# Kernel optimization log

Hardware: AMD Instinct MI355X
Metric: run time of the kernel (lower is better)

The kernel has to match this reference:

```python
import jax, jax.numpy as jnp
import numpy as np

EMBED = 1024
HEADS = 16
HEAD_DIM = EMBED // HEADS


def setup_inputs() -> dict:
    key = jax.random.key(0)
    ks = jax.random.split(key, 8)
    N, S, E = 4, 2048, EMBED
    s = 1.0 / np.sqrt(E)
    return {
        "values": jax.random.normal(ks[0], (N, S, E), jnp.float32),
        "keys": jax.random.normal(ks[1], (N, S, E), jnp.float32),
        "queries": jax.random.normal(ks[2], (N, S, E), jnp.float32),
        # nn.Linear weights stored as (out_features, in_features)
        "Wv": jax.random.normal(ks[3], (E, E), jnp.float32) * s,
        "Wk": jax.random.normal(ks[4], (E, E), jnp.float32) * s,
        "Wq": jax.random.normal(ks[5], (E, E), jnp.float32) * s,
        "Wo": jax.random.normal(ks[6], (E, E), jnp.float32) * s,
        "bo": jax.random.normal(ks[7], (E,), jnp.float32) * s,
    }


def reference(values, keys, queries, Wv, Wk, Wq, Wo, bo):
    N = queries.shape[0]
    H, D, E = HEADS, HEAD_DIM, EMBED
    # projections (torch Linear: x @ W.T), reshape to [N, S, H, D]
    v = (values @ Wv.T).reshape(N, -1, H, D)
    k = (keys @ Wk.T).reshape(N, -1, H, D)
    q = (queries @ Wq.T).reshape(N, -1, H, D)
    energy = jnp.einsum("nqhd,nkhd->nhqk", q, k)
    # NOTE: original scales by sqrt(embed_size), not sqrt(head_dim)
    attn = jax.nn.softmax(energy / jnp.sqrt(jnp.float32(E)), axis=3)
    out = jnp.einsum("nhql,nlhd->nqhd", attn, v).reshape(N, -1, H * D)
    return out @ Wo.T + bo
```

## Files before the change

### kernel.cpp

```cpp
#include <hip/hip_runtime.h>

typedef __bf16  bf16x8 __attribute__((ext_vector_type(8)));
typedef __bf16  bf16x4 __attribute__((ext_vector_type(4)));
typedef short   s16x4  __attribute__((ext_vector_type(4)));
typedef float   f32x4  __attribute__((ext_vector_type(4)));
typedef unsigned short u16x8 __attribute__((ext_vector_type(8)));

__device__ __forceinline__ unsigned short f2bf(float f) {
    union { float f; unsigned int u; } v; v.f = f;
    unsigned int u = v.u;
    unsigned int r = (u + 0x7fffu + ((u >> 16) & 1u)) >> 16;
    return (unsigned short)r;
}

__device__ __forceinline__ unsigned int pkbf(float lo, float hi) {
    union { float f; unsigned int u; } a, b; a.f = lo; b.f = hi;
    return __builtin_amdgcn_perm(b.u + 0x8000u, a.u + 0x8000u, 0x07060302u);
}

__device__ __forceinline__ void gld_lds16(const unsigned short* g, unsigned short* l) {
    auto gp = (const __attribute__((address_space(1))) unsigned int*)(const void*)g;
    auto lp = (__attribute__((address_space(3))) unsigned int*)(unsigned int)(unsigned long long)(void*)l;
    __builtin_amdgcn_global_load_lds(gp, lp, 16, 0, 0);
}

__device__ __forceinline__ f32x4 mfma16(bf16x4 a, bf16x4 b, f32x4 c) {
#if __has_builtin(__builtin_amdgcn_mfma_f32_16x16x16_bf16)
    return __builtin_amdgcn_mfma_f32_16x16x16_bf16(a, b, c, 0, 0, 0);
#elif __has_builtin(__builtin_amdgcn_mfma_f32_16x16x16bf16_1k)
    union U { bf16x4 h; s16x4 s; } ua, ub; ua.h = a; ub.h = b;
    return __builtin_amdgcn_mfma_f32_16x16x16bf16_1k(ua.s, ub.s, c, 0, 0, 0);
#else
    asm("v_mfma_f32_16x16x16_bf16 %0, %1, %2, %0" : "+v"(c) : "v"(a), "v"(b));
    return c;
#endif
}

__global__ void cast4_kernel(const float* __restrict__ a, const float* __restrict__ b,
                             const float* __restrict__ c, const float* __restrict__ d,
                             unsigned short* __restrict__ dst) {
    int sel = blockIdx.x >> 10;
    int off4 = (blockIdx.x & 1023) * 256 + threadIdx.x;
    const float* src = sel == 0 ? a : sel == 1 ? b : sel == 2 ? c : d;
    float4 f = ((const float4*)src)[off4];
    uint2 pk; pk.x = pkbf(f.x, f.y); pk.y = pkbf(f.z, f.w);
    ((uint2*)(dst + (size_t)sel * 1048576))[off4] = pk;
}

__global__ void cast_kernel(const float* __restrict__ src, unsigned short* __restrict__ dst, int n4) {
    int stride = gridDim.x * 256;
    for (int i = blockIdx.x * 256 + threadIdx.x; i < n4; i += stride) {
        float4 f = ((const float4*)src)[i];
        uint2 pk; pk.x = pkbf(f.x, f.y); pk.y = pkbf(f.z, f.w);
        ((uint2*)dst)[i] = pk;
    }
}

template <int MODE>
__global__ __launch_bounds__(256, 3)
void gemm_bt(const unsigned short* __restrict__ A, const unsigned short* __restrict__ Bt,
             void* __restrict__ dst, const float* __restrict__ bias, float a_scale)
{
    constexpr int K = 1024;
    __shared__ unsigned short As[2][4096];
    __shared__ unsigned short Bs[2][4096];

    const int t    = threadIdx.x;
    const int lane = t & 63;
    const int w    = t >> 6;
    const int q    = lane >> 4;
    const int ln   = lane & 15;
    const int wr   = w >> 1, wc = w & 1;
    const int m0   = blockIdx.x * 128;
    const int n0   = blockIdx.y * 128;
    const int srow = lane >> 2;
    const int scol = (lane & 3) * 8;

    f32x4 acc[4][4];
    const f32x4 zz = {0.f, 0.f, 0.f, 0.f};
#pragma unroll
    for (int i = 0; i < 4; ++i)
#pragma unroll
        for (int j = 0; j < 4; ++j) acc[i][j] = zz;

    auto stage = [&](int k0, int p) {
#pragma unroll
        for (int c = 0; c < 2; ++c) {
            int u = w * 2 + c;
            gld_lds16(A  + (size_t)(m0 + u * 16 + srow) * K + k0 + scol, &As[p][u * 512]);
            gld_lds16(Bt + (size_t)(n0 + u * 16 + srow) * K + k0 + scol, &Bs[p][u * 512]);
        }
    };

    stage(0, 0);
    for (int j = 0; j < 32; ++j) {
        __syncthreads();
        if (j < 31) stage((j + 1) * 32, (j + 1) & 1);
        const int p = j & 1;
        bf16x8 af[4], bfr[4];
#pragma unroll
        for (int i = 0; i < 4; ++i)
            af[i] = *(const bf16x8*)&As[p][(wr * 64 + i * 16 + ln) * 32 + q * 8];
#pragma unroll
        for (int jj = 0; jj < 4; ++jj)
            bfr[jj] = *(const bf16x8*)&Bs[p][(wc * 64 + jj * 16 + ln) * 32 + q * 8];
#pragma unroll
        for (int i = 0; i < 4; ++i)
#pragma unroll
            for (int jj = 0; jj < 4; ++jj)
                acc[i][jj] = __builtin_amdgcn_mfma_f32_16x16x32_bf16(af[i], bfr[jj], acc[i][jj], 0, 0, 0);
    }

#pragma unroll
    for (int i = 0; i < 4; ++i) {
#pragma unroll
        for (int j = 0; j < 4; ++j) {
            f32x4 c = acc[i][j];
            int mb = m0 + wr * 64 + i * 16 + q * 4;
            int nn = n0 + wc * 64 + j * 16 + ln;
            if constexpr (MODE == 1) {
                int b = mb >> 11, s = mb & 2047, h = nn >> 6, d = nn & 63;
                uint2 pk;
                pk.x = pkbf(c[0], c[1]);
                pk.y = pkbf(c[2], c[3]);
                size_t idx = (((size_t)(b * 16 + h) * 64) + d) * 2048 + s;
                *(uint2*)&((unsigned short*)dst)[idx] = pk;
            } else {
#pragma unroll
                for (int r = 0; r < 4; ++r) {
                    int m = mb + r;
                    float val = c[r] * a_scale;
                    if constexpr (MODE == 2) {
                        ((float*)dst)[(size_t)m * 1024 + nn] = val + bias[nn];
                    } else {
                        int b = m >> 11, s = m & 2047, h = nn >> 6, d = nn & 63;
                        size_t idx = (((size_t)(b * 16 + h) * 2048) + s) * 64 + d;
                        ((unsigned short*)dst)[idx] = f2bf(val);
                    }
                }
            }
        }
    }
}

__global__ __launch_bounds__(256, 4)
void attn_kernel(const unsigned short* __restrict__ Q, const unsigned short* __restrict__ Kg,
                 const unsigned short* __restrict__ Vt, unsigned short* __restrict__ Og)
{
    __shared__ __align__(16) unsigned short Ks[2][4096];
    __shared__ __align__(16) unsigned short Vs[2][4096];

    const int t    = threadIdx.x;
    const int lane = t & 63;
    const int w    = t >> 6;
    const int q    = lane >> 4;
    const int ln   = lane & 15;
    const int xs   = (ln >> 1) & 3;
    const int head = blockIdx.x;
    const int qt   = blockIdx.y;

    const unsigned short* Qh  = Q  + (size_t)head * 2048 * 64;
    const unsigned short* Kh  = Kg + (size_t)head * 2048 * 64;
    const unsigned short* Vth = Vt + (size_t)head * 64 * 2048;

    const int srow = lane >> 2;
    const int ssw  = ((lane & 3) ^ ((lane >> 3) & 3)) * 8;

    bf16x8 qf[2][2];
    const int rowb = qt * 128 + w * 32;
#pragma unroll
    for (int ti = 0; ti < 2; ++ti)
#pragma unroll
        for (int kc = 0; kc < 2; ++kc)
            qf[ti][kc] = *(const bf16x8*)&Qh[(size_t)(rowb + ti * 16 + ln) * 64 + kc * 32 + q * 8];

    const f32x4 zz = {0.f, 0.f, 0.f, 0.f};
    f32x4 oa[2][4];
#pragma unroll
    for (int ti = 0; ti < 2; ++ti)
#pragma unroll
        for (int dt = 0; dt < 4; ++dt) oa[ti][dt] = zz;
    float l_s[2] = {0.f, 0.f};

    auto stage = [&](int j, int p) {
#pragma unroll
        for (int c = 0; c < 2; ++c) {
            int u = w * 2 + c;
            int kc = u >> 2, rg = u & 3;
            gld_lds16(Kh + (size_t)(j * 64 + rg * 16 + srow) * 64 + kc * 32 + ssw,
                      &Ks[p][kc * 2048 + rg * 512]);
            gld_lds16(Vth + (size_t)(rg * 16 + srow) * 2048 + j * 64 + kc * 32 + ssw,
                      &Vs[p][kc * 2048 + rg * 512]);
        }
    };

    stage(0, 0);
    for (int j = 0; j < 32; ++j) {
        __syncthreads();
        if (j < 31) stage(j + 1, (j + 1) & 1);
        const int p = j & 1;

        bf16x4 pb[4][2];
        float rs0 = 0.f, rs1 = 0.f;
#pragma unroll
        for (int kt = 0; kt < 4; ++kt) {
            f32x4 s0 = zz, s1 = zz;
#pragma unroll
            for (int kc = 0; kc < 2; ++kc) {
                bf16x8 ka = *(const bf16x8*)&Ks[p][kc * 2048 + (kt * 16 + ln) * 32 + ((q ^ xs) * 8)];
                s0 = __builtin_amdgcn_mfma_f32_16x16x32_bf16(ka, qf[0][kc], s0, 0, 0, 0);
                s1 = __builtin_amdgcn_mfma_f32_16x16x32_bf16(ka, qf[1][kc], s1, 0, 0, 0);
            }
            {
                float a0 = exp2f(s0[0]), a1 = exp2f(s0[1]), a2 = exp2f(s0[2]), a3 = exp2f(s0[3]);
                rs0 += (a0 + a1) + (a2 + a3);
                f32x4 pe = {a0, a1, a2, a3};
                pb[kt][0] = __builtin_convertvector(pe, bf16x4);
            }
            {
                float b0 = exp2f(s1[0]), b1 = exp2f(s1[1]), b2 = exp2f(s1[2]), b3 = exp2f(s1[3]);
                rs1 += (b0 + b1) + (b2 + b3);
                f32x4 pe = {b0, b1, b2, b3};
                pb[kt][1] = __builtin_convertvector(pe, bf16x4);
            }
        }
        rs0 += __shfl_xor(rs0, 16); rs0 += __shfl_xor(rs0, 32); l_s[0] += rs0;
        rs1 += __shfl_xor(rs1, 16); rs1 += __shfl_xor(rs1, 32); l_s[1] += rs1;

#pragma unroll
        for (int kt = 0; kt < 4; ++kt) {
            const int kc = kt >> 1;
            const int so = ((((kt & 1) * 2 + (q >> 1)) ^ xs) * 8) + (q & 1) * 4;
            bf16x4 va[4];
#pragma unroll
            for (int dt = 0; dt < 4; ++dt)
                va[dt] = *(const bf16x4*)&Vs[p][kc * 2048 + (dt * 16 + ln) * 32 + so];
#pragma unroll
            for (int dt = 0; dt < 4; ++dt) {
                oa[0][dt] = mfma16(va[dt], pb[kt][0], oa[0][dt]);
                oa[1][dt] = mfma16(va[dt], pb[kt][1], oa[1][dt]);
            }
        }
    }

    const int n = head >> 4;
    const int hbase = (head & 15) * 64;
#pragma unroll
    for (int ti = 0; ti < 2; ++ti) {
        float inv = 1.f / l_s[ti];
        int sr = qt * 128 + w * 32 + ti * 16 + ln;
        size_t base = ((size_t)n * 2048 + sr) * 1024 + hbase;
#pragma unroll
        for (int dt = 0; dt < 4; ++dt) {
            uint2 pk;
            pk.x = pkbf(oa[ti][dt][0] * inv, oa[ti][dt][1] * inv);
            pk.y = pkbf(oa[ti][dt][2] * inv, oa[ti][dt][3] * inv);
            *(uint2*)&Og[base + dt * 16 + q * 4] = pk;
        }
    }
}

extern "C" void kernel_launch(void* const* d_in, const int* in_sizes, int n_in,
                              void* d_out, int out_size, void* d_ws, size_t ws_size,
                              hipStream_t stream)
{
    (void)in_sizes; (void)n_in; (void)out_size; (void)ws_size;
    const float* values  = (const float*)d_in[0];
    const float* keys    = (const float*)d_in[1];
    const float* queries = (const float*)d_in[2];
    const float* Wv = (const float*)d_in[3];
    const float* Wk = (const float*)d_in[4];
    const float* Wq = (const float*)d_in[5];
    const float* Wo = (const float*)d_in[6];
    const float* bo = (const float*)d_in[7];
    float* out = (float*)d_out;

    unsigned short* ws   = (unsigned short*)d_ws;
    unsigned short* Wv_b = ws;
    unsigned short* Wk_b = ws + 1048576;
    unsigned short* Wq_b = ws + 2097152;
    unsigned short* Wo_b = ws + 3145728;
    unsigned short* Act  = ws + 4194304;
    unsigned short* Ob   = Act;
    unsigned short* Qb   = ws + 12582912;
    unsigned short* Kb   = Qb + 8388608;
    unsigned short* Vtb  = Kb + 8388608;

    cast4_kernel<<<4096, 256, 0, stream>>>(Wv, Wk, Wq, Wo, ws);

    dim3 g(64, 8), b(256);
    const float qscale = 1.4426950408889634f / 32.f;

    cast_kernel<<<4096, 256, 0, stream>>>(values, Act, 2097152);
    gemm_bt<1><<<g, b, 0, stream>>>(Act, Wv_b, Vtb, nullptr, 1.f);
    cast_kernel<<<4096, 256, 0, stream>>>(keys, Act, 2097152);
    gemm_bt<0><<<g, b, 0, stream>>>(Act, Wk_b, Kb, nullptr, 1.f);
    cast_kernel<<<4096, 256, 0, stream>>>(queries, Act, 2097152);
    gemm_bt<0><<<g, b, 0, stream>>>(Act, Wq_b, Qb, nullptr, qscale);

    attn_kernel<<<dim3(64, 16), b, 0, stream>>>(Qb, Kb, Vtb, Ob);
    gemm_bt<2><<<g, b, 0, stream>>>(Ob, Wo_b, out, bo, 1.f);
}
```

Baseline: 367.6 us.

## Fuse fp32-to-bf16 activation casts into a single batched QKV projection GEMM

The three separate cast kernels and three projection GEMMs are replaced by one launch over a z-dimension of three. That kernel loads fp32 activations directly into registers and converts them to bf16 while staging into LDS, which removes the intermediate bf16 activation buffer and its round trip through memory. The attention kernel now uses the hardware exp2 builtin instead of exp2f, and it moves the cross-lane row-sum shuffles out of the inner loop so they run once at the end. In exchange, the A-operand path now goes through registers instead of the asynchronous global-to-LDS copy, which increases register pressure and may expose load latency.

Result: faster. 343.1 us (-6.7%).

```diff
diff --git a/kernel.cpp b/kernel.cpp
--- a/kernel.cpp
+++ b/kernel.cpp
@@ -4,7 +4,6 @@
 typedef __bf16  bf16x4 __attribute__((ext_vector_type(4)));
 typedef short   s16x4  __attribute__((ext_vector_type(4)));
 typedef float   f32x4  __attribute__((ext_vector_type(4)));
-typedef unsigned short u16x8 __attribute__((ext_vector_type(8)));
 
 __device__ __forceinline__ unsigned short f2bf(float f) {
     union { float f; unsigned int u; } v; v.f = f;
@@ -16,6 +15,14 @@
 __device__ __forceinline__ unsigned int pkbf(float lo, float hi) {
     union { float f; unsigned int u; } a, b; a.f = lo; b.f = hi;
     return __builtin_amdgcn_perm(b.u + 0x8000u, a.u + 0x8000u, 0x07060302u);
+}
+
+__device__ __forceinline__ float fexp2(float x) {
+#if __has_builtin(__builtin_amdgcn_exp2f)
+    return __builtin_amdgcn_exp2f(x);
+#else
+    float r; asm("v_exp_f32 %0, %1\n\ts_nop 1" : "=v"(r) : "v"(x)); return r;
+#endif
 }
 
 __device__ __forceinline__ void gld_lds16(const unsigned short* g, unsigned short* l) {
@@ -47,23 +54,21 @@
     ((uint2*)(dst + (size_t)sel * 1048576))[off4] = pk;
 }
 
-__global__ void cast_kernel(const float* __restrict__ src, unsigned short* __restrict__ dst, int n4) {
-    int stride = gridDim.x * 256;
-    for (int i = blockIdx.x * 256 + threadIdx.x; i < n4; i += stride) {
-        float4 f = ((const float4*)src)[i];
-        uint2 pk; pk.x = pkbf(f.x, f.y); pk.y = pkbf(f.z, f.w);
-        ((uint2*)dst)[i] = pk;
-    }
-}
-
-template <int MODE>
 __global__ __launch_bounds__(256, 3)
-void gemm_bt(const unsigned short* __restrict__ A, const unsigned short* __restrict__ Bt,
-             void* __restrict__ dst, const float* __restrict__ bias, float a_scale)
+void gemm_qkv(const float* __restrict__ V32, const float* __restrict__ K32,
+              const float* __restrict__ Q32, const unsigned short* __restrict__ W,
+              unsigned short* __restrict__ Vtb, unsigned short* __restrict__ Kb,
+              unsigned short* __restrict__ Qb, float qscale)
 {
     constexpr int K = 1024;
     __shared__ unsigned short As[2][4096];
     __shared__ unsigned short Bs[2][4096];
+
+    const int z = blockIdx.z;
+    const float* A32 = z == 0 ? V32 : z == 1 ? K32 : Q32;
+    const unsigned short* Bt = W + (size_t)z * 1048576;
+    unsigned short* dst = z == 0 ? Vtb : z == 1 ? Kb : Qb;
+    const float a_scale = z == 2 ? qscale : 1.f;
 
     const int t    = threadIdx.x;
     const int lane = t & 63;
@@ -83,6 +88,113 @@
 #pragma unroll
         for (int j = 0; j < 4; ++j) acc[i][j] = zz;
 
+    auto loadA = [&](int k0, float4* fa) {
+#pragma unroll
+        for (int c = 0; c < 2; ++c) {
+            int u = w * 2 + c;
+            const float* src = A32 + (size_t)(m0 + u * 16 + srow) * K + k0 + scol;
+            fa[c * 2]     = *(const float4*)src;
+            fa[c * 2 + 1] = *(const float4*)(src + 4);
+        }
+    };
+    auto writeA = [&](const float4* fa, int p) {
+#pragma unroll
+        for (int c = 0; c < 2; ++c) {
+            int u = w * 2 + c;
+            uint4 pk;
+            pk.x = pkbf(fa[c * 2].x,     fa[c * 2].y);
+            pk.y = pkbf(fa[c * 2].z,     fa[c * 2].w);
+            pk.z = pkbf(fa[c * 2 + 1].x, fa[c * 2 + 1].y);
+            pk.w = pkbf(fa[c * 2 + 1].z, fa[c * 2 + 1].w);
+            *(uint4*)&As[p][u * 512 + lane * 8] = pk;
+        }
+    };
+    auto stageB = [&](int k0, int p) {
+#pragma unroll
+        for (int c = 0; c < 2; ++c) {
+            int u = w * 2 + c;
+            gld_lds16(Bt + (size_t)(n0 + u * 16 + srow) * K + k0 + scol, &Bs[p][u * 512]);
+        }
+    };
+
+    float4 fa[4];
+    loadA(0, fa);
+    stageB(0, 0);
+    writeA(fa, 0);
+    for (int j = 0; j < 32; ++j) {
+        __syncthreads();
+        if (j < 31) { loadA((j + 1) * 32, fa); stageB((j + 1) * 32, (j + 1) & 1); }
+        const int p = j & 1;
+        bf16x8 af[4], bfr[4];
+#pragma unroll
+        for (int i = 0; i < 4; ++i)
+            af[i] = *(const bf16x8*)&As[p][(wr * 64 + i * 16 + ln) * 32 + q * 8];
+#pragma unroll
+        for (int jj = 0; jj < 4; ++jj)
+            bfr[jj] = *(const bf16x8*)&Bs[p][(wc * 64 + jj * 16 + ln) * 32 + q * 8];
+#pragma unroll
+        for (int i = 0; i < 4; ++i)
+#pragma unroll
+            for (int jj = 0; jj < 4; ++jj)
+                acc[i][jj] = __builtin_amdgcn_mfma_f32_16x16x32_bf16(af[i], bfr[jj], acc[i][jj], 0, 0, 0);
+        if (j < 31) writeA(fa, (j + 1) & 1);
+    }
+
+#pragma unroll
+    for (int i = 0; i < 4; ++i) {
+#pragma unroll
+        for (int jj = 0; jj < 4; ++jj) {
+            f32x4 c = acc[i][jj];
+            int mb = m0 + wr * 64 + i * 16 + q * 4;
+            int nn = n0 + wc * 64 + jj * 16 + ln;
+            if (z == 0) {
+                int b = mb >> 11, s = mb & 2047, h = nn >> 6, d = nn & 63;
+                uint2 pk;
+                pk.x = pkbf(c[0], c[1]);
+                pk.y = pkbf(c[2], c[3]);
+                size_t idx = (((size_t)(b * 16 + h) * 64) + d) * 2048 + s;
+                *(uint2*)&dst[idx] = pk;
+            } else {
+#pragma unroll
+                for (int r = 0; r < 4; ++r) {
+                    int m = mb + r;
+                    float val = c[r] * a_scale;
+                    int b = m >> 11, s = m & 2047, h = nn >> 6, d = nn & 63;
+                    size_t idx = (((size_t)(b * 16 + h) * 2048) + s) * 64 + d;
+                    dst[idx] = f2bf(val);
+                }
+            }
+        }
+    }
+}
+
+template <int MODE>
+__global__ __launch_bounds__(256, 3)
+void gemm_bt(const unsigned short* __restrict__ A, const unsigned short* __restrict__ Bt,
+             void* __restrict__ dst, const float* __restrict__ bias, float a_scale)
+{
+    constexpr int K = 1024;
+    __shared__ unsigned short As[2][4096];
+    __shared__ unsigned short Bs[2][4096];
+
+    const int t    = threadIdx.x;
+    const int lane = t & 63;
+    const int w    = t >> 6;
+    const int q    = lane >> 4;
+    const int ln   = lane & 15;
+    const int wr   = w >> 1, wc = w & 1;
+    const int m0   = blockIdx.x * 128;
+    const int n0   = blockIdx.y * 128;
+    const int srow = lane >> 2;
+    const int scol = (lane & 3) * 8;
+
+    f32x4 acc[4][4];
+    const f32x4 zz = {0.f, 0.f, 0.f, 0.f};
+#pragma unroll
+    for (int i = 0; i < 4; ++i)
+#pragma unroll
+        for (int j = 0; j < 4; ++j) acc[i][j] = zz;
+
     auto stage = [&](int k0, int p) {
 #pragma unroll
         for (int c = 0; c < 2; ++c) {
@@ -118,26 +230,11 @@
             f32x4 c = acc[i][j];
             int mb = m0 + wr * 64 + i * 16 + q * 4;
             int nn = n0 + wc * 64 + j * 16 + ln;
-            if constexpr (MODE == 1) {
-                int b = mb >> 11, s = mb & 2047, h = nn >> 6, d = nn & 63;
-                uint2 pk;
-                pk.x = pkbf(c[0], c[1]);
-                pk.y = pkbf(c[2], c[3]);
-                size_t idx = (((size_t)(b * 16 + h) * 64) + d) * 2048 + s;
-                *(uint2*)&((unsigned short*)dst)[idx] = pk;
-            } else {
-#pragma unroll
-                for (int r = 0; r < 4; ++r) {
-                    int m = mb + r;
-                    float val = c[r] * a_scale;
-                    if constexpr (MODE == 2) {
-                        ((float*)dst)[(size_t)m * 1024 + nn] = val + bias[nn];
-                    } else {
-                        int b = m >> 11, s = m & 2047, h = nn >> 6, d = nn & 63;
-                        size_t idx = (((size_t)(b * 16 + h) * 2048) + s) * 64 + d;
-                        ((unsigned short*)dst)[idx] = f2bf(val);
-                    }
-                }
+#pragma unroll
+            for (int r = 0; r < 4; ++r) {
+                int m = mb + r;
+                float val = c[r] * a_scale;
+                ((float*)dst)[(size_t)m * 1024 + nn] = val + bias[nn];
             }
         }
     }
@@ -212,20 +309,20 @@
                 s1 = __builtin_amdgcn_mfma_f32_16x16x32_bf16(ka, qf[1][kc], s1, 0, 0, 0);
             }
             {
-                float a0 = exp2f(s0[0]), a1 = exp2f(s0[1]), a2 = exp2f(s0[2]), a3 = exp2f(s0[3]);
+                float a0 = fexp2(s0[0]), a1 = fexp2(s0[1]), a2 = fexp2(s0[2]), a3 = fexp2(s0[3]);
                 rs0 += (a0 + a1) + (a2 + a3);
                 f32x4 pe = {a0, a1, a2, a3};
                 pb[kt][0] = __builtin_convertvector(pe, bf16x4);
             }
             {
-                float b0 = exp2f(s1[0]), b1 = exp2f(s1[1]), b2 = exp2f(s1[2]), b3 = exp2f(s1[3]);
+                float b0 = fexp2(s1[0]), b1 = fexp2(s1[1]), b2 = fexp2(s1[2]), b3 = fexp2(s1[3]);
                 rs1 += (b0 + b1) + (b2 + b3);
                 f32x4 pe = {b0, b1, b2, b3};
                 pb[kt][1] = __builtin_convertvector(pe, bf16x4);
             }
         }
-        rs0 += __shfl_xor(rs0, 16); rs0 += __shfl_xor(rs0, 32); l_s[0] += rs0;
-        rs1 += __shfl_xor(rs1, 16); rs1 += __shfl_xor(rs1, 32); l_s[1] += rs1;
+        l_s[0] += rs0;
+        l_s[1] += rs1;
 
 #pragma unroll
         for (int kt = 0; kt < 4; ++kt) {
@@ -242,6 +339,9 @@
             }
         }
     }
+
+    l_s[0] += __shfl_xor(l_s[0], 16); l_s[0] += __shfl_xor(l_s[0], 32);
+    l_s[1] += __shfl_xor(l_s[1], 16); l_s[1] += __shfl_xor(l_s[1], 32);
 
     const int n = head >> 4;
     const int hbase = (head & 15) * 64;
@@ -276,28 +376,17 @@
     float* out = (float*)d_out;
 
     unsigned short* ws   = (unsigned short*)d_ws;
-    unsigned short* Wv_b = ws;
-    unsigned short* Wk_b = ws + 1048576;
-    unsigned short* Wq_b = ws + 2097152;
     unsigned short* Wo_b = ws + 3145728;
-    unsigned short* Act  = ws + 4194304;
-    unsigned short* Ob   = Act;
+    unsigned short* Ob   = ws + 4194304;
     unsigned short* Qb   = ws + 12582912;
     unsigned short* Kb   = Qb + 8388608;
     unsigned short* Vtb  = Kb + 8388608;
 
-    cast4_kernel<<<4096, 256, 0, stream>>>(Wv, Wk, Wq, Wo, ws);
-
-    dim3 g(64, 8), b(256);
     const float qscale = 1.4426950408889634f / 32.f;
-
-    cast_kernel<<<4096, 256, 0, stream>>>(values, Act, 2097152);
-    gemm_bt<1><<<g, b, 0, stream>>>(Act, Wv_b, Vtb, nullptr, 1.f);
-    cast_kernel<<<4096, 256, 0, stream>>>(keys, Act, 2097152);
-    gemm_bt<0><<<g, b, 0, stream>>>(Act, Wk_b, Kb, nullptr, 1.f);
-    cast_kernel<<<4096, 256, 0, stream>>>(queries, Act, 2097152);
-    gemm_bt<0><<<g, b, 0, stream>>>(Act, Wq_b, Qb, nullptr, qscale);
-
+    dim3 b(256);
+
+    cast4_kernel<<<4096, b, 0, stream>>>(Wv, Wk, Wq, Wo, ws);
+    gemm_qkv<<<dim3(64, 8, 3), b, 0, stream>>>(values, keys, queries, ws, Vtb, Kb, Qb, qscale);
     attn_kernel<<<dim3(64, 16), b, 0, stream>>>(Qb, Kb, Vtb, Ob);
-    gemm_bt<2><<<g, b, 0, stream>>>(Ob, Wo_b, out, bo, 1.f);
-}
+    gemm_bt<2><<<dim3(64, 8), b, 0, stream>>>(Ob, Wo_b, out, bo, 1.f);
+}
```
